# Kernel optimization log

Measured on AMD Instinct MI355X. Metric: run time of the kernel, lower is better.

Reference implementation:

```python
import jax, jax.numpy as jnp
import numpy as np

B, H, S, D = 2, 12, 3456, 32
FEATS_PER_T = 216
WINDOW_LEN = 8
ACT_SIZE = 16
IMG_FEAT_SIZE = 196
DECODER_ONLY = False


def eye_mask(seq_len, feats_per_t, window_len, act_size, img_feat_size, decoder_only=False):
    """Boolean [S, S] mask replicating get_eye_block_mask's memory_mask."""
    idx = jnp.arange(seq_len)
    q_t = (idx // feats_per_t)[:, None]          # [S,1]
    kv_t = (idx // feats_per_t)[None, :]         # [1,S]
    q_m = (idx % feats_per_t)[:, None]
    kv_m = (idx % feats_per_t)[None, :]
    proprio_idx_mod = 2 + 1 + 1
    img_start = feats_per_t - img_feat_size
    joint_start = img_start - act_size

    causal = (q_t >= kv_t) & (q_t - kv_t < window_len)
    is_q_img = q_m >= img_start
    is_kv_img = kv_m >= img_start
    is_q_joint = (q_m >= joint_start) & (q_m < img_start)
    is_kv_joint = (kv_m >= joint_start) & (kv_m < img_start)
    is_kv_proprio = kv_m == proprio_idx_mod

    img_to_img = ~(is_q_img & is_kv_img)
    same_t = q_t == kv_t
    joint_past_joint = ~(is_q_joint & is_kv_joint & ~same_t)
    proprio_past = ~(is_kv_proprio & (kv_t < q_t))
    past_image = ~(is_kv_img & (kv_t < q_t))
    m = causal & img_to_img & joint_past_joint & proprio_past & past_image
    if decoder_only:
        m = m & ~(is_q_img & ~is_kv_img)
    return m


def setup_inputs() -> dict:
    key = jax.random.key(0)
    kq, kk, kv = jax.random.split(key, 3)
    return {
        "q": jax.random.normal(kq, (B, H, S, D), dtype=jnp.float32),
        "k": jax.random.normal(kk, (B, H, S, D), dtype=jnp.float32),
        "v": jax.random.normal(kv, (B, H, S, D), dtype=jnp.float32),
        "feats_per_t": FEATS_PER_T,
        "window_len": WINDOW_LEN,
        "act_size": ACT_SIZE,
        "img_feat_size": IMG_FEAT_SIZE,
    }


def reference(q, k, v, feats_per_t, window_len, act_size, img_feat_size):
    seq_len = q.shape[2]
    mask = eye_mask(seq_len, feats_per_t, window_len, act_size,
                    img_feat_size, DECODER_ONLY)  # [S,S]
    scale = 1.0 / jnp.sqrt(jnp.array(q.shape[-1], q.dtype))
    scores = jnp.einsum("bhqd,bhkd->bhqk", q, k) * scale
    neg = jnp.asarray(jnp.finfo(scores.dtype).min, scores.dtype)
    scores = jnp.where(mask[None, None], scores, neg)
    attn = jax.nn.softmax(scores, axis=-1)
    return jnp.einsum("bhqk,bhkd->bhqd", attn, v)
```

## Files before the change

kernel.cpp:

```cpp
#include <hip/hip_runtime.h>

#define SEQ   3456
#define DH    32
#define FPT   216
#define NT    16
#define IMG0  20
#define SCALE 0.17677669529663687f

#define KPAD   40
#define VPAD   168
#define PPITCH 40

typedef __attribute__((ext_vector_type(8))) short bf16x8;
typedef __attribute__((ext_vector_type(4))) float f32x4;

#define MFMA16(a,b,c) __builtin_amdgcn_mfma_f32_16x16x32_bf16(a,b,c,0,0,0)

__device__ __forceinline__ unsigned short bfh(float f) {
    unsigned u = __float_as_uint(f);
    u += 0x7FFFu + ((u >> 16) & 1u);
    return (unsigned short)(u >> 16);
}
__device__ __forceinline__ float bff(unsigned short h) {
    return __uint_as_float((unsigned)h << 16);
}
__device__ __forceinline__ void split8(const float* f, bf16x8& hi, bf16x8& lo) {
    #pragma unroll
    for (int j = 0; j < 8; ++j) {
        unsigned short h = bfh(f[j]);
        hi[j] = (short)h;
        lo[j] = (short)bfh(f[j] - bff(h));
    }
}

__constant__ unsigned MN_TAB[5] = {0xFEFFFFFFu, 0xFFFFEFFFu, 0xFFEFFFFEu,
                                   0xEFFFFEFFu, 0xFFFEFFFFu};
__constant__ unsigned MJ_TAB[5] = {0x00FFFFFFu, 0xF0000F00u, 0x000F0000u,
                                   0x0F0000F0u, 0x0000F000u};

__global__ __launch_bounds__(256)
void eye_attn_mfma3(const float* __restrict__ q, const float* __restrict__ k,
                    const float* __restrict__ v, float* __restrict__ out) {
    __shared__ __align__(16) unsigned short KsHi[160 * KPAD];
    __shared__ __align__(16) unsigned short VtHi[DH * VPAD];
    __shared__ __align__(16) unsigned short Pu[8 * 16 * PPITCH];

    const int t = blockIdx.x, bh = blockIdx.y, half = blockIdx.z;
    const int tid = threadIdx.x;
    const size_t base = (size_t)bh * SEQ * DH;
    const int dmax = (t < 7) ? t : 7;
    const int nkeys = IMG0 * (dmax + 1);

    for (int i = tid; i < 160 * 8; i += 256) {
        const int g = i >> 3, c = i & 7;
        float4 kk = make_float4(0.f,0.f,0.f,0.f), vv = make_float4(0.f,0.f,0.f,0.f);
        if (g < nkeys) {
            const int d = g / IMG0, jj = g - d * IMG0;
            const size_t row = base + (size_t)((t - d) * FPT + jj) * DH + c * 4;
            kk = *(const float4*)(k + row);
            vv = *(const float4*)(v + row);
        }
        const float kf[4] = {kk.x, kk.y, kk.z, kk.w};
        const float vf[4] = {vv.x, vv.y, vv.z, vv.w};
        ushort4 khi;
        unsigned short* ah = (unsigned short*)&khi;
        #pragma unroll
        for (int e = 0; e < 4; ++e) ah[e] = bfh(kf[e]);
        *(ushort4*)(KsHi + g * KPAD + c * 4) = khi;
        #pragma unroll
        for (int e = 0; e < 4; ++e)
            VtHi[(c * 4 + e) * VPAD + g] = bfh(vf[e]);
    }
    __syncthreads();

    const int wv = tid >> 6, lane = tid & 63;
    const int col = lane & 15, quad = lane >> 4;

    unsigned mNt[5], mJt[5];
    #pragma unroll
    for (int kt = 0; kt < 5; ++kt) {
        const int tr = nkeys - kt * 32;
        unsigned mn = MN_TAB[kt], mj = MJ_TAB[kt];
        if (tr <= 0) { mn = 0u; mj = 0u; }
        else if (tr < 32) { const unsigned lim = (1u << tr) - 1u; mn &= lim; mj &= lim; }
        mNt[kt] = mn; mJt[kt] = mj;
    }

    int mt[2]; int mcnt; bool do_img = false;
    if (half == 0) {
        if (wv == 0)      { mt[0] = 0; mcnt = 1; do_img = true; }
        else if (wv == 1) { mt[0] = 1; mcnt = 1; do_img = true; }
        else if (wv == 2) { mt[0] = 2; mt[1] = 3; mcnt = 2; }
        else              { mt[0] = 4; mt[1] = 5; mcnt = 2; }
    } else {
        mt[0] = 6 + 2 * wv; mt[1] = 7 + 2 * wv; mcnt = 2;
    }

    bf16x8 bones;
    #pragma unroll
    for (int j = 0; j < 8; ++j) bones[j] = (short)(col == 0 ? 0x3F80 : 0);

    for (int mi = 0; mi < mcnt; ++mi) {
        const int mb = mt[mi] * 16;
        bf16x8 qhi, qlo;
        {
            const int qc = min(mb + col, FPT - 1);
            const float* qp = q + base + (size_t)(t * FPT + qc) * DH + quad * 8;
            float qf[8];
            const float4 a0 = *(const float4*)qp;
            const float4 a1 = *(const float4*)(qp + 4);
            qf[0]=a0.x*SCALE; qf[1]=a0.y*SCALE; qf[2]=a0.z*SCALE; qf[3]=a0.w*SCALE;
            qf[4]=a1.x*SCALE; qf[5]=a1.y*SCALE; qf[6]=a1.z*SCALE; qf[7]=a1.w*SCALE;
            split8(qf, qhi, qlo);
        }
        f32x4 oacc0 = {0.f,0.f,0.f,0.f}, oacc1 = {0.f,0.f,0.f,0.f};
        f32x4 lacc = {0.f,0.f,0.f,0.f};

        #pragma unroll
        for (int kt = 0; kt < 5; ++kt) {
            unsigned short* myP = Pu + (wv * 2 + (kt & 1)) * 16 * PPITCH;
            f32x4 s[2];
            #pragma unroll
            for (int h = 0; h < 2; ++h) {
                const int key = kt * 32 + h * 16 + col;
                const bf16x8 khi = *(const bf16x8*)(KsHi + key * KPAD + quad * 8);
                f32x4 acc = {0.f,0.f,0.f,0.f};
                acc = MFMA16(qhi, khi, acc);
                acc = MFMA16(qlo, khi, acc);
                s[h] = acc;
            }
            #pragma unroll
            for (int r = 0; r < 4; ++r) {
                const int qm = mb + quad * 4 + r;
                const bool isj = (qm >= 4) && (qm < IMG0);
                const unsigned m = (qm < FPT) ? (isj ? mJt[kt] : mNt[kt]) : 0u;
                #pragma unroll
                for (int h = 0; h < 2; ++h) {
                    const float e = ((m >> (h * 16 + col)) & 1u)
                                    ? __expf(s[h][r]) : 0.f;
                    myP[(quad * 4 + r) * PPITCH + h * 16 + col] = bfh(e);
                }
            }
            const bf16x8 phi = *(const bf16x8*)(myP + col * PPITCH + quad * 8);
            #pragma unroll
            for (int h = 0; h < 2; ++h) {
                const int dim = h * 16 + col;
                const bf16x8 vhi = *(const bf16x8*)(VtHi + dim * VPAD + kt * 32 + quad * 8);
                f32x4& oa = h ? oacc1 : oacc0;
                oa = MFMA16(phi, vhi, oa);
            }
            lacc = MFMA16(phi, bones, lacc);
        }

        if (mi == 0 && do_img) {
            for (int kt2 = 0; kt2 < 7; ++kt2) {
                unsigned short* myP = Pu + (wv * 2 + (kt2 & 1)) * 16 * PPITCH;
                f32x4 s[2];
                #pragma unroll
                for (int h = 0; h < 2; ++h) {
                    const int keyc = min(IMG0 + kt2 * 32 + h * 16 + col, FPT - 1);
                    const float* kp = k + base + (size_t)(t * FPT + keyc) * DH + quad * 8;
                    float kf[8];
                    const float4 a0 = *(const float4*)kp;
                    const float4 a1 = *(const float4*)(kp + 4);
                    kf[0]=a0.x; kf[1]=a0.y; kf[2]=a0.z; kf[3]=a0.w;
                    kf[4]=a1.x; kf[5]=a1.y; kf[6]=a1.z; kf[7]=a1.w;
                    bf16x8 khi;
                    #pragma unroll
                    for (int j = 0; j < 8; ++j) khi[j] = (short)bfh(kf[j]);
                    f32x4 acc = {0.f,0.f,0.f,0.f};
                    acc = MFMA16(qhi, khi, acc);
                    acc = MFMA16(qlo, khi, acc);
                    s[h] = acc;
                }
                #pragma unroll
                for (int h = 0; h < 2; ++h) {
                    const int key = IMG0 + kt2 * 32 + h * 16 + col;
                    #pragma unroll
                    for (int r = 0; r < 4; ++r) {
                        const int qm = mb + quad * 4 + r;
                        const bool vis = (key < FPT) && (qm < IMG0);
                        const float e = vis ? __expf(s[h][r]) : 0.f;
                        myP[(quad * 4 + r) * PPITCH + h * 16 + col] = bfh(e);
                    }
                }
                const bf16x8 phi = *(const bf16x8*)(myP + col * PPITCH + quad * 8);
                #pragma unroll
                for (int h = 0; h < 2; ++h) {
                    const int dim = h * 16 + col;
                    float vf[8];
                    #pragma unroll
                    for (int j = 0; j < 8; ++j) {
                        const int ky = min(IMG0 + kt2 * 32 + quad * 8 + j, FPT - 1);
                        vf[j] = v[base + (size_t)(t * FPT + ky) * DH + dim];
                    }
                    bf16x8 vhi;
                    #pragma unroll
                    for (int j = 0; j < 8; ++j) vhi[j] = (short)bfh(vf[j]);
                    f32x4& oa = h ? oacc1 : oacc0;
                    oa = MFMA16(phi, vhi, oa);
                }
                lacc = MFMA16(phi, bones, lacc);
            }
        }

        #pragma unroll
        for (int r = 0; r < 4; ++r) {
            const float lr = __shfl(lacc[r], lane & 48);
            const float inv = 1.f / lr;
            const int qm = mb + quad * 4 + r;
            if (qm < FPT) {
                float* op = out + base + (size_t)(t * FPT + qm) * DH;
                op[col]      = oacc0[r] * inv;
                op[16 + col] = oacc1[r] * inv;
            }
        }
    }
}

extern "C" void kernel_launch(void* const* d_in, const int* in_sizes, int n_in,
                              void* d_out, int out_size, void* d_ws, size_t ws_size,
                              hipStream_t stream) {
    const float* q = (const float*)d_in[0];
    const float* k = (const float*)d_in[1];
    const float* v = (const float*)d_in[2];
    float* out = (float*)d_out;
    const int BH = in_sizes[0] / (SEQ * DH);
    dim3 grid(NT, BH, 2);
    eye_attn_mfma3<<<grid, 256, 0, stream>>>(q, k, v, out);
}
```

Measured before the change: 100.9 us.

## Split image-key work across waves and stage image V in shared memory

Waves 0-1 of half 0 now compute only the intra-timestep image-key attention for query tiles 0-1. Waves 2-3 compute those tiles' shared-key part and pass partial sums through shared memory for a final merge. The remaining tiles are redistributed so each wave gets 2-3 tiles. Image V rows are staged transposed in shared memory as bf16, replacing strided scalar global gathers, and the key-tile loop is bounded by the actual number of shared keys. This balances per-wave work and cuts redundant global loads, at the cost of more LDS, an extra block barrier, and a larger staging loop.

```diff
diff --git a/kernel.cpp b/kernel.cpp
--- a/kernel.cpp
+++ b/kernel.cpp
@@ -9,6 +9,7 @@
 
 #define KPAD   40
 #define VPAD   168
+#define IPAD   232
 #define PPITCH 40
 
 typedef __attribute__((ext_vector_type(8))) short bf16x8;
@@ -39,37 +40,55 @@
                                    0x0F0000F0u, 0x0000F000u};
 
 __global__ __launch_bounds__(256)
-void eye_attn_mfma3(const float* __restrict__ q, const float* __restrict__ k,
+void eye_attn_mfma5(const float* __restrict__ q, const float* __restrict__ k,
                     const float* __restrict__ v, float* __restrict__ out) {
     __shared__ __align__(16) unsigned short KsHi[160 * KPAD];
     __shared__ __align__(16) unsigned short VtHi[DH * VPAD];
-    __shared__ __align__(16) unsigned short Pu[8 * 16 * PPITCH];
+    __shared__ __align__(16) unsigned short VtImg[DH * IPAD];
+    __shared__ __align__(16) unsigned short Pu[4 * 16 * PPITCH];
+    __shared__ float Mg[2][64][13];
 
     const int t = blockIdx.x, bh = blockIdx.y, half = blockIdx.z;
     const int tid = threadIdx.x;
     const size_t base = (size_t)bh * SEQ * DH;
     const int dmax = (t < 7) ? t : 7;
     const int nkeys = IMG0 * (dmax + 1);
-
-    for (int i = tid; i < 160 * 8; i += 256) {
-        const int g = i >> 3, c = i & 7;
-        float4 kk = make_float4(0.f,0.f,0.f,0.f), vv = make_float4(0.f,0.f,0.f,0.f);
-        if (g < nkeys) {
-            const int d = g / IMG0, jj = g - d * IMG0;
-            const size_t row = base + (size_t)((t - d) * FPT + jj) * DH + c * 4;
-            kk = *(const float4*)(k + row);
-            vv = *(const float4*)(v + row);
-        }
-        const float kf[4] = {kk.x, kk.y, kk.z, kk.w};
-        const float vf[4] = {vv.x, vv.y, vv.z, vv.w};
-        ushort4 khi;
-        unsigned short* ah = (unsigned short*)&khi;
-        #pragma unroll
-        for (int e = 0; e < 4; ++e) ah[e] = bfh(kf[e]);
-        *(ushort4*)(KsHi + g * KPAD + c * 4) = khi;
-        #pragma unroll
-        for (int e = 0; e < 4; ++e)
-            VtHi[(c * 4 + e) * VPAD + g] = bfh(vf[e]);
+    const int nkt = (nkeys + 31) >> 5;
+
+    for (int i = tid; i < 3072; i += 256) {
+        if (i < 1280) {
+            const int g = i >> 3, c = i & 7;
+            float4 kk = make_float4(0.f,0.f,0.f,0.f);
+            float4 vv = make_float4(0.f,0.f,0.f,0.f);
+            if (g < nkeys) {
+                const int d = g / IMG0, jj = g - d * IMG0;
+                const size_t row = base + (size_t)((t - d) * FPT + jj) * DH + c * 4;
+                kk = *(const float4*)(k + row);
+                vv = *(const float4*)(v + row);
+            }
+            const float kf[4] = {kk.x, kk.y, kk.z, kk.w};
+            const float vf[4] = {vv.x, vv.y, vv.z, vv.w};
+            ushort4 khi;
+            unsigned short* ah = (unsigned short*)&khi;
+            #pragma unroll
+            for (int e = 0; e < 4; ++e) ah[e] = bfh(kf[e]);
+            *(ushort4*)(KsHi + g * KPAD + c * 4) = khi;
+            #pragma unroll
+            for (int e = 0; e < 4; ++e)
+                VtHi[(c * 4 + e) * VPAD + g] = bfh(vf[e]);
+        } else {
+            const int ii = i - 1280;
+            const int gi = ii >> 3, c = ii & 7;
+            float4 vv = make_float4(0.f,0.f,0.f,0.f);
+            if (gi < 196) {
+                const size_t row = base + (size_t)(t * FPT + IMG0 + gi) * DH + c * 4;
+                vv = *(const float4*)(v + row);
+            }
+            const float vf[4] = {vv.x, vv.y, vv.z, vv.w};
+            #pragma unroll
+            for (int e = 0; e < 4; ++e)
+                VtImg[(c * 4 + e) * IPAD + gi] = bfh(vf[e]);
+        }
     }
     __syncthreads();
 
@@ -86,22 +105,29 @@
         mNt[kt] = mn; mJt[kt] = mj;
     }
 
-    int mt[2]; int mcnt; bool do_img = false;
-    if (half == 0) {
-        if (wv == 0)      { mt[0] = 0; mcnt = 1; do_img = true; }
-        else if (wv == 1) { mt[0] = 1; mcnt = 1; do_img = true; }
-        else if (wv == 2) { mt[0] = 2; mt[1] = 3; mcnt = 2; }
-        else              { mt[0] = 4; mt[1] = 5; mcnt = 2; }
-    } else {
-        mt[0] = 6 + 2 * wv; mt[1] = 7 + 2 * wv; mcnt = 2;
-    }
-
     bf16x8 bones;
     #pragma unroll
     for (int j = 0; j < 8; ++j) bones[j] = (short)(col == 0 ? 0x3F80 : 0);
 
-    for (int mi = 0; mi < mcnt; ++mi) {
-        const int mb = mt[mi] * 16;
+    unsigned short* myP = Pu + wv * 16 * PPITCH;
+
+    const bool isImgWave = (half == 0) && (wv < 2);
+
+    int tl[3]; int ntile = 0;
+    if (half == 0) {
+        if (wv >= 2) { tl[0] = wv - 2; tl[1] = wv; ntile = 2; }
+    } else {
+        if (wv == 0)      { tl[0]=4;  tl[1]=5;  tl[2]=6; ntile = 3; }
+        else if (wv == 1) { tl[0]=7;  tl[1]=8;  tl[2]=9; ntile = 3; }
+        else if (wv == 2) { tl[0]=10; tl[1]=11; ntile = 2; }
+        else              { tl[0]=12; tl[1]=13; ntile = 2; }
+    }
+
+    f32x4 ioacc0 = {0.f,0.f,0.f,0.f}, ioacc1 = {0.f,0.f,0.f,0.f};
+    f32x4 ilacc  = {0.f,0.f,0.f,0.f};
+
+    if (isImgWave) {
+        const int mb = wv * 16;
         bf16x8 qhi, qlo;
         {
             const int qc = min(mb + col, FPT - 1);
@@ -113,31 +139,33 @@
             qf[4]=a1.x*SCALE; qf[5]=a1.y*SCALE; qf[6]=a1.z*SCALE; qf[7]=a1.w*SCALE;
             split8(qf, qhi, qlo);
         }
-        f32x4 oacc0 = {0.f,0.f,0.f,0.f}, oacc1 = {0.f,0.f,0.f,0.f};
-        f32x4 lacc = {0.f,0.f,0.f,0.f};
-
-        #pragma unroll
-        for (int kt = 0; kt < 5; ++kt) {
-            unsigned short* myP = Pu + (wv * 2 + (kt & 1)) * 16 * PPITCH;
+        for (int kt2 = 0; kt2 < 7; ++kt2) {
             f32x4 s[2];
             #pragma unroll
             for (int h = 0; h < 2; ++h) {
-                const int key = kt * 32 + h * 16 + col;
-                const bf16x8 khi = *(const bf16x8*)(KsHi + key * KPAD + quad * 8);
+                const int keyc = min(IMG0 + kt2 * 32 + h * 16 + col, FPT - 1);
+                const float* kp = k + base + (size_t)(t * FPT + keyc) * DH + quad * 8;
+                float kf[8];
+                const float4 a0 = *(const float4*)kp;
+                const float4 a1 = *(const float4*)(kp + 4);
+                kf[0]=a0.x; kf[1]=a0.y; kf[2]=a0.z; kf[3]=a0.w;
+                kf[4]=a1.x; kf[5]=a1.y; kf[6]=a1.z; kf[7]=a1.w;
+                bf16x8 khi;
+                #pragma unroll
+                for (int j = 0; j < 8; ++j) khi[j] = (short)bfh(kf[j]);
                 f32x4 acc = {0.f,0.f,0.f,0.f};
                 acc = MFMA16(qhi, khi, acc);
                 acc = MFMA16(qlo, khi, acc);
                 s[h] = acc;
             }
             #pragma unroll
-            for (int r = 0; r < 4; ++r) {
-                const int qm = mb + quad * 4 + r;
-                const bool isj = (qm >= 4) && (qm < IMG0);
-                const unsigned m = (qm < FPT) ? (isj ? mJt[kt] : mNt[kt]) : 0u;
-                #pragma unroll
-                for (int h = 0; h < 2; ++h) {
-                    const float e = ((m >> (h * 16 + col)) & 1u)
-                                    ? __expf(s[h][r]) : 0.f;
+            for (int h = 0; h < 2; ++h) {
+                const int key = IMG0 + kt2 * 32 + h * 16 + col;
+                #pragma unroll
+                for (int r = 0; r < 4; ++r) {
+                    const int qm = mb + quad * 4 + r;
+                    const bool vis = (key < FPT) && (qm < IMG0);
+                    const float e = vis ? __expf(s[h][r]) : 0.f;
                     myP[(quad * 4 + r) * PPITCH + h * 16 + col] = bfh(e);
                 }
             }
@@ -145,42 +173,48 @@
             #pragma unroll
             for (int h = 0; h < 2; ++h) {
                 const int dim = h * 16 + col;
-                const bf16x8 vhi = *(const bf16x8*)(VtHi + dim * VPAD + kt * 32 + quad * 8);
-                f32x4& oa = h ? oacc1 : oacc0;
+                const bf16x8 vhi = *(const bf16x8*)(VtImg + dim * IPAD + kt2 * 32 + quad * 8);
+                f32x4& oa = h ? ioacc1 : ioacc0;
                 oa = MFMA16(phi, vhi, oa);
             }
-            lacc = MFMA16(phi, bones, lacc);
-        }
-
-        if (mi == 0 && do_img) {
-            for (int kt2 = 0; kt2 < 7; ++kt2) {
-                unsigned short* myP = Pu + (wv * 2 + (kt2 & 1)) * 16 * PPITCH;
+            ilacc = MFMA16(phi, bones, ilacc);
+        }
+    } else {
+        for (int mi = 0; mi < ntile; ++mi) {
+            const int mb = tl[mi] * 16;
+            bf16x8 qhi, qlo;
+            {
+                const int qc = min(mb + col, FPT - 1);
+                const float* qp = q + base + (size_t)(t * FPT + qc) * DH + quad * 8;
+                float qf[8];
+                const float4 a0 = *(const float4*)qp;
+                const float4 a1 = *(const float4*)(qp + 4);
+                qf[0]=a0.x*SCALE; qf[1]=a0.y*SCALE; qf[2]=a0.z*SCALE; qf[3]=a0.w*SCALE;
+                qf[4]=a1.x*SCALE; qf[5]=a1.y*SCALE; qf[6]=a1.z*SCALE; qf[7]=a1.w*SCALE;
+                split8(qf, qhi, qlo);
+            }
+            f32x4 oacc0 = {0.f,0.f,0.f,0.f}, oacc1 = {0.f,0.f,0.f,0.f};
+            f32x4 lacc = {0.f,0.f,0.f,0.f};
+            for (int kt = 0; kt < nkt; ++kt) {
                 f32x4 s[2];
                 #pragma unroll
                 for (int h = 0; h < 2; ++h) {
-                    const int keyc = min(IMG0 + kt2 * 32 + h * 16 + col, FPT - 1);
-                    const float* kp = k + base + (size_t)(t * FPT + keyc) * DH + quad * 8;
-                    float kf[8];
-                    const float4 a0 = *(const float4*)kp;
-                    const float4 a1 = *(const float4*)(kp + 4);
-                    kf[0]=a0.x; kf[1]=a0.y; kf[2]=a0.z; kf[3]=a0.w;
-                    kf[4]=a1.x; kf[5]=a1.y; kf[6]=a1.z; kf[7]=a1.w;
-                    bf16x8 khi;
-                    #pragma unroll
-                    for (int j = 0; j < 8; ++j) khi[j] = (short)bfh(kf[j]);
+                    const int key = kt * 32 + h * 16 + col;
+                    const bf16x8 khi = *(const bf16x8*)(KsHi + key * KPAD + quad * 8);
                     f32x4 acc = {0.f,0.f,0.f,0.f};
                     acc = MFMA16(qhi, khi, acc);
                     acc = MFMA16(qlo, khi, acc);
                     s[h] = acc;
                 }
                 #pragma unroll
-                for (int h = 0; h < 2; ++h) {
-                    const int key = IMG0 + kt2 * 32 + h * 16 + col;
+                for (int r = 0; r < 4; ++r) {
+                    const int qm = mb + quad * 4 + r;
+                    const bool isj = (qm >= 4) && (qm < IMG0);
+                    const unsigned m = (qm < FPT) ? (isj ? mJt[kt] : mNt[kt]) : 0u;
                     #pragma unroll
-                    for (int r = 0; r < 4; ++r) {
-                        const int qm = mb + quad * 4 + r;
-                        const bool vis = (key < FPT) && (qm < IMG0);
-                        const float e = vis ? __expf(s[h][r]) : 0.f;
+                    for (int h = 0; h < 2; ++h) {
+                        const float e = ((m >> (h * 16 + col)) & 1u)
+                                        ? __expf(s[h][r]) : 0.f;
                         myP[(quad * 4 + r) * PPITCH + h * 16 + col] = bfh(e);
                     }
                 }
@@ -188,31 +222,57 @@
                 #pragma unroll
                 for (int h = 0; h < 2; ++h) {
                     const int dim = h * 16 + col;
-                    float vf[8];
-                    #pragma unroll
-                    for (int j = 0; j < 8; ++j) {
-                        const int ky = min(IMG0 + kt2 * 32 + quad * 8 + j, FPT - 1);
-                        vf[j] = v[base + (size_t)(t * FPT + ky) * DH + dim];
-                    }
-                    bf16x8 vhi;
-                    #pragma unroll
-                    for (int j = 0; j < 8; ++j) vhi[j] = (short)bfh(vf[j]);
+                    const bf16x8 vhi = *(const bf16x8*)(VtHi + dim * VPAD + kt * 32 + quad * 8);
                     f32x4& oa = h ? oacc1 : oacc0;
                     oa = MFMA16(phi, vhi, oa);
                 }
                 lacc = MFMA16(phi, bones, lacc);
             }
-        }
-
-        #pragma unroll
-        for (int r = 0; r < 4; ++r) {
-            const float lr = __shfl(lacc[r], lane & 48);
-            const float inv = 1.f / lr;
-            const int qm = mb + quad * 4 + r;
-            if (qm < FPT) {
-                float* op = out + base + (size_t)(t * FPT + qm) * DH;
-                op[col]      = oacc0[r] * inv;
-                op[16 + col] = oacc1[r] * inv;
+            if (half == 0 && mi == 0) {
+                float* mp = &Mg[wv - 2][lane][0];
+                #pragma unroll
+                for (int r = 0; r < 4; ++r) {
+                    mp[r]     = lacc[r];
+                    mp[4 + r] = oacc0[r];
+                    mp[8 + r] = oacc1[r];
+                }
+            } else {
+                #pragma unroll
+                for (int r = 0; r < 4; ++r) {
+                    const float lr = __shfl(lacc[r], lane & 48);
+                    const float inv = 1.f / lr;
+                    const int qm = mb + quad * 4 + r;
+                    if (qm < FPT) {
+                        float* op = out + base + (size_t)(t * FPT + qm) * DH;
+                        op[col]      = oacc0[r] * inv;
+                        op[16 + col] = oacc1[r] * inv;
+                    }
+                }
+            }
+        }
+    }
+
+    if (half == 0) {
+        __syncthreads();
+        if (wv < 2) {
+            const float* mp = &Mg[wv][lane][0];
+            #pragma unroll
+            for (int r = 0; r < 4; ++r) {
+                ilacc[r]  += mp[r];
+                ioacc0[r] += mp[4 + r];
+                ioacc1[r] += mp[8 + r];
+            }
+            const int mb = wv * 16;
+            #pragma unroll
+            for (int r = 0; r < 4; ++r) {
+                const float lr = __shfl(ilacc[r], lane & 48);
+                const float inv = 1.f / lr;
+                const int qm = mb + quad * 4 + r;
+                if (qm < FPT) {
+                    float* op = out + base + (size_t)(t * FPT + qm) * DH;
+                    op[col]      = ioacc0[r] * inv;
+                    op[16 + col] = ioacc1[r] * inv;
+                }
             }
         }
     }
@@ -227,5 +287,5 @@
     float* out = (float*)d_out;
     const int BH = in_sizes[0] / (SEQ * DH);
     dim3 grid(NT, BH, 2);
-    eye_attn_mfma3<<<grid, 256, 0, stream>>>(q, k, v, out);
-}
+    eye_attn_mfma5<<<grid, 256, 0, stream>>>(q, k, v, out);
+}
```

Result: no change. 101.8 us (+0.8%).

## Stage image V block in shared memory, trim key tiles, use exp2 scaling

Applied to the files above, without the earlier changes.

Image-key V values for the current timestep are now loaded once per block into a transposed bf16 shared buffer (half 0 only). Previously each wave read them as scattered strided scalar global loads inside the image loop. The non-image key loop now runs only over the key tiles actually present (nkt) instead of a fixed 5, and staging skips padded keys, zeroing only the V tail. Softmax folds log2(e) into the Q scale so it can use exp2f, and the P buffer drops to a single slot per wave, with some extra shared memory and staging work in exchange.

```diff
diff --git a/kernel.cpp b/kernel.cpp
--- a/kernel.cpp
+++ b/kernel.cpp
@@ -5,10 +5,11 @@
 #define FPT   216
 #define NT    16
 #define IMG0  20
-#define SCALE 0.17677669529663687f
+#define SCALE2 0.2550707067f
 
 #define KPAD   40
 #define VPAD   168
+#define IPAD   232
 #define PPITCH 40
 
 typedef __attribute__((ext_vector_type(8))) short bf16x8;
@@ -39,27 +40,26 @@
                                    0x0F0000F0u, 0x0000F000u};
 
 __global__ __launch_bounds__(256)
-void eye_attn_mfma3(const float* __restrict__ q, const float* __restrict__ k,
+void eye_attn_mfma6(const float* __restrict__ q, const float* __restrict__ k,
                     const float* __restrict__ v, float* __restrict__ out) {
     __shared__ __align__(16) unsigned short KsHi[160 * KPAD];
     __shared__ __align__(16) unsigned short VtHi[DH * VPAD];
-    __shared__ __align__(16) unsigned short Pu[8 * 16 * PPITCH];
+    __shared__ __align__(16) unsigned short VtImg[DH * IPAD];
+    __shared__ __align__(16) unsigned short Pu[4 * 16 * PPITCH];
 
     const int t = blockIdx.x, bh = blockIdx.y, half = blockIdx.z;
     const int tid = threadIdx.x;
     const size_t base = (size_t)bh * SEQ * DH;
     const int dmax = (t < 7) ? t : 7;
     const int nkeys = IMG0 * (dmax + 1);
-
-    for (int i = tid; i < 160 * 8; i += 256) {
+    const int nkt = (nkeys + 31) >> 5;
+
+    for (int i = tid; i < nkeys * 8; i += 256) {
         const int g = i >> 3, c = i & 7;
-        float4 kk = make_float4(0.f,0.f,0.f,0.f), vv = make_float4(0.f,0.f,0.f,0.f);
-        if (g < nkeys) {
-            const int d = g / IMG0, jj = g - d * IMG0;
-            const size_t row = base + (size_t)((t - d) * FPT + jj) * DH + c * 4;
-            kk = *(const float4*)(k + row);
-            vv = *(const float4*)(v + row);
-        }
+        const int d = g / IMG0, jj = g - d * IMG0;
+        const size_t row = base + (size_t)((t - d) * FPT + jj) * DH + c * 4;
+        const float4 kk = *(const float4*)(k + row);
+        const float4 vv = *(const float4*)(v + row);
         const float kf[4] = {kk.x, kk.y, kk.z, kk.w};
         const float vf[4] = {vv.x, vv.y, vv.z, vv.w};
         ushort4 khi;
@@ -71,6 +71,30 @@
         for (int e = 0; e < 4; ++e)
             VtHi[(c * 4 + e) * VPAD + g] = bfh(vf[e]);
     }
+    {
+        const int rem = nkeys - (nkt - 1) * 32;
+        if (rem < 32) {
+            for (int i = tid; i < 1024; i += 256) {
+                const int c = i & 31;
+                if (c >= rem)
+                    VtHi[(i >> 5) * VPAD + (nkt - 1) * 32 + c] = 0;
+            }
+        }
+    }
+    if (half == 0) {
+        for (int i = tid; i < 1792; i += 256) {
+            const int gi = i >> 3, c = i & 7;
+            float4 vv = make_float4(0.f, 0.f, 0.f, 0.f);
+            if (gi < 196) {
+                const size_t row = base + (size_t)(t * FPT + IMG0 + gi) * DH + c * 4;
+                vv = *(const float4*)(v + row);
+            }
+            const float vf[4] = {vv.x, vv.y, vv.z, vv.w};
+            #pragma unroll
+            for (int e = 0; e < 4; ++e)
+                VtImg[(c * 4 + e) * IPAD + gi] = bfh(vf[e]);
+        }
+    }
     __syncthreads();
 
     const int wv = tid >> 6, lane = tid & 63;
@@ -86,6 +110,12 @@
         mNt[kt] = mn; mJt[kt] = mj;
     }
 
+    bf16x8 bones;
+    #pragma unroll
+    for (int j = 0; j < 8; ++j) bones[j] = (short)(col == 0 ? 0x3F80 : 0);
+
+    unsigned short* myP = Pu + wv * 16 * PPITCH;
+
     int mt[2]; int mcnt; bool do_img = false;
     if (half == 0) {
         if (wv == 0)      { mt[0] = 0; mcnt = 1; do_img = true; }
@@ -95,10 +125,6 @@
     } else {
         mt[0] = 6 + 2 * wv; mt[1] = 7 + 2 * wv; mcnt = 2;
     }
-
-    bf16x8 bones;
-    #pragma unroll
-    for (int j = 0; j < 8; ++j) bones[j] = (short)(col == 0 ? 0x3F80 : 0);
 
     for (int mi = 0; mi < mcnt; ++mi) {
         const int mb = mt[mi] * 16;
@@ -109,16 +135,14 @@
             float qf[8];
             const float4 a0 = *(const float4*)qp;
             const float4 a1 = *(const float4*)(qp + 4);
-            qf[0]=a0.x*SCALE; qf[1]=a0.y*SCALE; qf[2]=a0.z*SCALE; qf[3]=a0.w*SCALE;
-            qf[4]=a1.x*SCALE; qf[5]=a1.y*SCALE; qf[6]=a1.z*SCALE; qf[7]=a1.w*SCALE;
+            qf[0]=a0.x*SCALE2; qf[1]=a0.y*SCALE2; qf[2]=a0.z*SCALE2; qf[3]=a0.w*SCALE2;
+            qf[4]=a1.x*SCALE2; qf[5]=a1.y*SCALE2; qf[6]=a1.z*SCALE2; qf[7]=a1.w*SCALE2;
             split8(qf, qhi, qlo);
         }
         f32x4 oacc0 = {0.f,0.f,0.f,0.f}, oacc1 = {0.f,0.f,0.f,0.f};
         f32x4 lacc = {0.f,0.f,0.f,0.f};
 
-        #pragma unroll
-        for (int kt = 0; kt < 5; ++kt) {
-            unsigned short* myP = Pu + (wv * 2 + (kt & 1)) * 16 * PPITCH;
+        for (int kt = 0; kt < nkt; ++kt) {
             f32x4 s[2];
             #pragma unroll
             for (int h = 0; h < 2; ++h) {
@@ -137,7 +161,7 @@
                 #pragma unroll
                 for (int h = 0; h < 2; ++h) {
                     const float e = ((m >> (h * 16 + col)) & 1u)
-                                    ? __expf(s[h][r]) : 0.f;
+                                    ? exp2f(s[h][r]) : 0.f;
                     myP[(quad * 4 + r) * PPITCH + h * 16 + col] = bfh(e);
                 }
             }
@@ -154,7 +178,6 @@
 
         if (mi == 0 && do_img) {
             for (int kt2 = 0; kt2 < 7; ++kt2) {
-                unsigned short* myP = Pu + (wv * 2 + (kt2 & 1)) * 16 * PPITCH;
                 f32x4 s[2];
                 #pragma unroll
                 for (int h = 0; h < 2; ++h) {
@@ -180,7 +203,7 @@
                     for (int r = 0; r < 4; ++r) {
                         const int qm = mb + quad * 4 + r;
                         const bool vis = (key < FPT) && (qm < IMG0);
-                        const float e = vis ? __expf(s[h][r]) : 0.f;
+                        const float e = vis ? exp2f(s[h][r]) : 0.f;
                         myP[(quad * 4 + r) * PPITCH + h * 16 + col] = bfh(e);
                     }
                 }
@@ -188,15 +211,7 @@
                 #pragma unroll
                 for (int h = 0; h < 2; ++h) {
                     const int dim = h * 16 + col;
-                    float vf[8];
-                    #pragma unroll
-                    for (int j = 0; j < 8; ++j) {
-                        const int ky = min(IMG0 + kt2 * 32 + quad * 8 + j, FPT - 1);
-                        vf[j] = v[base + (size_t)(t * FPT + ky) * DH + dim];
-                    }
-                    bf16x8 vhi;
-                    #pragma unroll
-                    for (int j = 0; j < 8; ++j) vhi[j] = (short)bfh(vf[j]);
+                    const bf16x8 vhi = *(const bf16x8*)(VtImg + dim * IPAD + kt2 * 32 + quad * 8);
                     f32x4& oa = h ? oacc1 : oacc0;
                     oa = MFMA16(phi, vhi, oa);
                 }
@@ -227,5 +242,5 @@
     float* out = (float*)d_out;
     const int BH = in_sizes[0] / (SEQ * DH);
     dim3 grid(NT, BH, 2);
-    eye_attn_mfma3<<<grid, 256, 0, stream>>>(q, k, v, out);
-}
+    eye_attn_mfma6<<<grid, 256, 0, stream>>>(q, k, v, out);
+}
```

New measurement: 99.14 us. No clear change (-1.8%).
